# Kernel tuning notes

Hardware: AMD Instinct MI355X
Metric: run time of the kernel (lower is better)

The kernel has to match this reference:

```python
import jax, jax.numpy as jnp
import numpy as np

B, T, V = 4, 2048, 2048
D = 256   # state_dim
R = 512   # inner_dim
EPS = float(jnp.finfo(jnp.float32).eps)  # F.rms_norm default eps = dtype eps


def rms_norm(x):
    return x * jax.lax.rsqrt(jnp.mean(x * x, axis=-1, keepdims=True) + EPS)


def setup_inputs() -> dict:
    key = jax.random.key(0)
    ks = jax.random.split(key, 9)
    std = 0.02
    return {
        "x": jax.random.normal(ks[0], (B, T, V), dtype=jnp.float32),
        "Wq": jax.random.normal(ks[1], (D, V), dtype=jnp.float32) * std,
        "Wk": jax.random.normal(ks[2], (D, V), dtype=jnp.float32) * std,
        "Wv": jax.random.normal(ks[3], (D, V), dtype=jnp.float32) * std,
        "Wo": jax.random.normal(ks[4], (V, D), dtype=jnp.float32) * std,
        "decay_logit": jnp.float32(3.0),
        "q_out_scale": jnp.float32(0.1),
        "Wdown": jax.random.normal(ks[5], (R, V), dtype=jnp.float32) * std,
        "Wup": jax.random.normal(ks[6], (V, R), dtype=jnp.float32) * std,
        "t_bias": jnp.zeros((R,), dtype=jnp.float32),
        "t_out_scale": jnp.float32(0.1),
        "q_scale": jnp.ones((1,), dtype=jnp.float32),
        "t_scale": jnp.ones((1,), dtype=jnp.float32),
    }


def qtable(x, Wq, Wk, Wv, Wo, decay_logit, out_scale):
    # x: (B,T,V)
    q = jnp.einsum('btv,dv->btd', x, Wq)
    k = jnp.einsum('btv,dv->btd', x, Wk)
    v = jnp.einsum('btv,dv->btd', x, Wv)
    scores = jnp.einsum('btd,bsd->bts', q, k)  # (B,T,T)
    decay = jax.nn.sigmoid(decay_logit)
    pos = jnp.arange(T)
    diff = pos[None, :] - pos[:, None]  # diff[t,s] = s - t ... matches torch (unsqueeze(0)-unsqueeze(1))
    causal = (diff > 0).astype(jnp.float32)
    weights = decay ** jnp.clip(diff.astype(jnp.float32) - 1.0, 0.0, None) * causal
    scores = scores * weights[None, :, :]
    retrieved = jnp.einsum('bts,bsd->btd', scores, v)
    return jnp.einsum('btd,vd->btv', retrieved, Wo) * out_scale


def transform(x, Wdown, Wup, bias, out_scale):
    h = jnp.einsum('btv,rv->btr', x, Wdown) + bias
    h = jax.nn.gelu(h, approximate=False)
    return jnp.einsum('btr,vr->btv', h, Wup) * out_scale


def reference(x, Wq, Wk, Wv, Wo, decay_logit, q_out_scale,
              Wdown, Wup, t_bias, t_out_scale, q_scale, t_scale):
    x = x + q_scale * qtable(rms_norm(x), Wq, Wk, Wv, Wo, decay_logit, q_out_scale)
    x = x + t_scale * transform(rms_norm(x), Wdown, Wup, t_bias, t_out_scale)
    return x
```

## Files before the change

kernel.cpp:

```cpp
#include <hip/hip_runtime.h>
#include <cmath>

typedef _Float16 f16;
typedef _Float16 f16x8 __attribute__((ext_vector_type(8)));
typedef _Float16 f16x4 __attribute__((ext_vector_type(4)));
typedef float f32x4 __attribute__((ext_vector_type(4)));

#define MFMA16(a, b, c) __builtin_amdgcn_mfma_f32_16x16x32_f16(a, b, c, 0, 0, 0)

static constexpr int Bsz = 4;
static constexpr int T = 2048;
static constexpr int V = 2048;
static constexpr int D = 256;
static constexpr int R = 512;
static constexpr int M = Bsz * T;

__device__ __forceinline__ void load_lds16(const f16* g, f16* l) {
    __builtin_amdgcn_global_load_lds(
        (const __attribute__((address_space(1))) unsigned int*)(unsigned long long)g,
        (__attribute__((address_space(3))) unsigned int*)(unsigned int)(unsigned long long)l,
        16, 0, 0);
}

__global__ __launch_bounds__(256) void conv_all(const float* __restrict__ s0,
                                                const float* __restrict__ s1,
                                                const float* __restrict__ s2,
                                                const float* __restrict__ s3,
                                                const float* __restrict__ s4,
                                                const float* __restrict__ s5,
                                                f16* __restrict__ dst) {
    int idx = (blockIdx.x * 256 + threadIdx.x) * 4;
    if (idx >= 4194304) return;
    const float* src; int off;
    if      (idx <  524288) { src = s0; off = idx; }
    else if (idx < 1048576) { src = s1; off = idx - 524288; }
    else if (idx < 1572864) { src = s2; off = idx - 1048576; }
    else if (idx < 2097152) { src = s3; off = idx - 1572864; }
    else if (idx < 3145728) { src = s4; off = idx - 2097152; }
    else                    { src = s5; off = idx - 3145728; }
    float4 v = *(const float4*)&src[off];
    f16x4 o;
    o[0] = (f16)v.x; o[1] = (f16)v.y; o[2] = (f16)v.z; o[3] = (f16)v.w;
    *(f16x4*)&dst[idx] = o;
}

__global__ __launch_bounds__(256) void rmsnorm_kernel(const float* __restrict__ x,
                                                      f16* __restrict__ out) {
    int row = blockIdx.x;
    const float* xr = x + (size_t)row * V;
    int tid = threadIdx.x;
    float4 v0 = ((const float4*)xr)[tid];
    float4 v1 = ((const float4*)xr)[tid + 256];
    float ss = v0.x * v0.x + v0.y * v0.y + v0.z * v0.z + v0.w * v0.w
             + v1.x * v1.x + v1.y * v1.y + v1.z * v1.z + v1.w * v1.w;
    #pragma unroll
    for (int o = 32; o > 0; o >>= 1) ss += __shfl_xor(ss, o);
    __shared__ float wsum[4];
    if ((tid & 63) == 0) wsum[tid >> 6] = ss;
    __syncthreads();
    float tot = wsum[0] + wsum[1] + wsum[2] + wsum[3];
    float s = rsqrtf(tot / (float)V + 1.1920929e-07f);
    f16* orow = out + (size_t)row * V;
    f16x4 o0, o1;
    o0[0] = (f16)(v0.x * s); o0[1] = (f16)(v0.y * s);
    o0[2] = (f16)(v0.z * s); o0[3] = (f16)(v0.w * s);
    o1[0] = (f16)(v1.x * s); o1[1] = (f16)(v1.y * s);
    o1[2] = (f16)(v1.z * s); o1[3] = (f16)(v1.w * s);
    *(f16x4*)&orow[tid * 4] = o0;
    *(f16x4*)&orow[1024 + tid * 4] = o1;
}

__global__ __launch_bounds__(256) void rmsnorm_f16(const f16* __restrict__ x,
                                                   f16* __restrict__ out) {
    int row = blockIdx.x;
    int tid = threadIdx.x;
    const f16* xr = x + (size_t)row * V;
    f16x8 v = *(const f16x8*)&xr[tid * 8];
    float f[8];
    float ss = 0.f;
    #pragma unroll
    for (int j = 0; j < 8; j++) { f[j] = (float)v[j]; ss += f[j] * f[j]; }
    #pragma unroll
    for (int o = 32; o > 0; o >>= 1) ss += __shfl_xor(ss, o);
    __shared__ float wsum[4];
    if ((tid & 63) == 0) wsum[tid >> 6] = ss;
    __syncthreads();
    float tot = wsum[0] + wsum[1] + wsum[2] + wsum[3];
    float s = rsqrtf(tot / (float)V + 1.1920929e-07f);
    f16x8 o;
    #pragma unroll
    for (int j = 0; j < 8; j++) o[j] = (f16)(f[j] * s);
    *(f16x8*)&out[(size_t)row * V + tid * 8] = o;
}

struct GemmEpi {
    const float* residf;
    const f16* residh;
    float* outf;
    f16* outh;
    f16* out_q; f16* out_k; f16* out_vT;
    f16* out_h;
    const float* bias;
    const float* sA; const float* sB;
};

template <int MODE>
__global__ __launch_bounds__(256) void gemm_nt(const f16* __restrict__ A,
                                               const f16* __restrict__ Bm,
                                               int K, GemmEpi e) {
    __shared__ f16 Asl[2][128 * 32];
    __shared__ f16 Bsl[2][128 * 32];
    int tid = threadIdx.x;
    int lane = tid & 63, wv = tid >> 6;
    int wm = wv >> 1, wn = wv & 1;
    int quad = lane >> 4, l16 = lane & 15;
    int m0 = blockIdx.x * 128, n0 = blockIdx.y * 128;
    f32x4 acc[4][4] = {};

    int srow = lane >> 2;
    int scg = (lane & 3) ^ ((lane >> 3) & 3);
    const f16* Ag0 = &A[(size_t)(m0 + 16 * wv + srow) * K + scg * 8];
    const f16* Ag1 = &A[(size_t)(m0 + 16 * (wv + 4) + srow) * K + scg * 8];
    const f16* Bg0 = &Bm[(size_t)(n0 + 16 * wv + srow) * K + scg * 8];
    const f16* Bg1 = &Bm[(size_t)(n0 + 16 * (wv + 4) + srow) * K + scg * 8];
    int lo0 = (16 * wv) * 32, lo1 = (16 * (wv + 4)) * 32;

    int fs = quad ^ ((l16 >> 1) & 3);
    int niter = K >> 5;

    load_lds16(Ag0, &Asl[0][lo0]);
    load_lds16(Ag1, &Asl[0][lo1]);
    load_lds16(Bg0, &Bsl[0][lo0]);
    load_lds16(Bg1, &Bsl[0][lo1]);

    for (int i = 0; i < niter; i++) {
        int cur = i & 1;
        __builtin_amdgcn_s_barrier();
        if (i + 1 < niter) {
            int k0 = (i + 1) << 5;
            int nb = cur ^ 1;
            load_lds16(Ag0 + k0, &Asl[nb][lo0]);
            load_lds16(Ag1 + k0, &Asl[nb][lo1]);
            load_lds16(Bg0 + k0, &Bsl[nb][lo0]);
            load_lds16(Bg1 + k0, &Bsl[nb][lo1]);
            asm volatile("s_waitcnt vmcnt(4)" ::: "memory");
        } else {
            asm volatile("s_waitcnt vmcnt(0)" ::: "memory");
        }
        __builtin_amdgcn_s_barrier();
        f16x8 af[4], bf[4];
        #pragma unroll
        for (int j = 0; j < 4; j++)
            af[j] = *(const f16x8*)&Asl[cur][(64 * wm + 16 * j + l16) * 32 + fs * 8];
        #pragma unroll
        for (int j = 0; j < 4; j++)
            bf[j] = *(const f16x8*)&Bsl[cur][(64 * wn + 16 * j + l16) * 32 + fs * 8];
        #pragma unroll
        for (int mi = 0; mi < 4; mi++)
            #pragma unroll
            for (int ni = 0; ni < 4; ni++)
                acc[mi][ni] = MFMA16(af[mi], bf[ni], acc[mi][ni]);
    }

    float s = 0.f;
    if (MODE == 1 || MODE == 3) s = e.sA[0] * e.sB[0];
    #pragma unroll
    for (int mi = 0; mi < 4; mi++) {
        #pragma unroll
        for (int ni = 0; ni < 4; ni++) {
            int ml = 64 * wm + 16 * mi + quad * 4;
            int nl = 64 * wn + 16 * ni + l16;
            int gn = n0 + nl;
            #pragma unroll
            for (int i = 0; i < 4; i++) {
                int gm = m0 + ml + i;
                float vv = acc[mi][ni][i];
                if (MODE == 0) {
                    if (gn < 256) {
                        e.out_q[(size_t)gm * D + gn] = (f16)vv;
                    } else if (gn < 512) {
                        e.out_k[(size_t)gm * D + (gn - 256)] = (f16)vv;
                    } else {
                        int d = gn - 512;
                        int b = gm >> 11, t = gm & 2047;
                        e.out_vT[((size_t)b * D + d) * T + t] = (f16)vv;
                    }
                } else if (MODE == 1) {
                    size_t o = (size_t)gm * V + gn;
                    e.outh[o] = (f16)(e.residf[o] + s * vv);
                } else if (MODE == 2) {
                    float z = vv + e.bias[gn];
                    float g = 0.5f * z * (1.f + erff(z * 0.70710678118654752f));
                    e.out_h[(size_t)gm * R + gn] = (f16)g;
                } else {
                    size_t o = (size_t)gm * V + gn;
                    e.outf[o] = (float)e.residh[o] + s * vv;
                }
            }
        }
    }
}

__global__ __launch_bounds__(256) void attn_kernel(const f16* __restrict__ q,
                                                   const f16* __restrict__ k,
                                                   const f16* __restrict__ vT,
                                                   f16* __restrict__ ret,
                                                   const float* __restrict__ decay_logit) {
    __shared__ f16 Ksl[64 * 264];
    __shared__ f16 Psl[64 * 72];
    int tid = threadIdx.x, lane = tid & 63, wv = tid >> 6;
    int quad = lane >> 4, l16 = lane & 15;
    int b = blockIdx.y, t0 = blockIdx.x * 64;
    const f16* qb = q + (size_t)b * T * D;
    const f16* kb = k + (size_t)b * T * D;
    const f16* vb = vT + (size_t)b * D * T;
    f16* rb = ret + (size_t)b * T * D;

    float dl = decay_logit[0];
    float decay = 1.f / (1.f + expf(-dl));
    float l2d = log2f(decay);
    float nl2d = -l2d;

    int tq = t0 + 16 * wv + l16;
    f16x8 qf[8];
    #pragma unroll
    for (int kk = 0; kk < 8; kk++)
        qf[kk] = *(const f16x8*)&qb[(size_t)tq * D + kk * 32 + quad * 8];

    f32x4 acc2[4][4] = {};

    for (int s0 = t0; s0 < T; s0 += 64) {
        if ((float)(s0 - t0 - 64) * nl2d > 25.f) break;
        __syncthreads();
        #pragma unroll
        for (int p = 0; p < 8; p++) {
            int e0 = p * 2048 + tid * 8;
            int rr = e0 >> 8, cc = e0 & 255;
            *(f16x8*)&Ksl[rr * 264 + cc] = *(const f16x8*)&kb[(size_t)(s0 + rr) * D + cc];
        }
        __syncthreads();
        f32x4 sacc[4] = {};
        #pragma unroll
        for (int ni = 0; ni < 4; ni++) {
            #pragma unroll
            for (int kk = 0; kk < 8; kk++) {
                f16x8 bf = *(const f16x8*)&Ksl[(16 * ni + l16) * 264 + kk * 32 + quad * 8];
                sacc[ni] = MFMA16(qf[kk], bf, sacc[ni]);
            }
        }
        #pragma unroll
        for (int ni = 0; ni < 4; ni++) {
            int s_ = s0 + 16 * ni + l16;
            #pragma unroll
            for (int i = 0; i < 4; i++) {
                int t_ = t0 + 16 * wv + quad * 4 + i;
                int diff = s_ - t_;
                float w = (diff > 0) ? exp2f((float)(diff - 1) * l2d) : 0.f;
                Psl[(16 * wv + quad * 4 + i) * 72 + 16 * ni + l16] = (f16)(sacc[ni][i] * w);
            }
        }
        __syncthreads();
        #pragma unroll
        for (int kk = 0; kk < 2; kk++) {
            f16x8 pa[4], vf[4];
            #pragma unroll
            for (int mi = 0; mi < 4; mi++)
                pa[mi] = *(const f16x8*)&Psl[(16 * mi + l16) * 72 + kk * 32 + quad * 8];
            #pragma unroll
            for (int ni = 0; ni < 4; ni++)
                vf[ni] = *(const f16x8*)&vb[(size_t)(64 * wv + 16 * ni + l16) * T + s0 + kk * 32 + quad * 8];
            #pragma unroll
            for (int mi = 0; mi < 4; mi++)
                #pragma unroll
                for (int ni = 0; ni < 4; ni++)
                    acc2[mi][ni] = MFMA16(pa[mi], vf[ni], acc2[mi][ni]);
        }
    }

    #pragma unroll
    for (int mi = 0; mi < 4; mi++) {
        #pragma unroll
        for (int ni = 0; ni < 4; ni++) {
            int t_ = t0 + 16 * mi + quad * 4;
            int d_ = 64 * wv + 16 * ni + l16;
            #pragma unroll
            for (int i = 0; i < 4; i++)
                rb[(size_t)(t_ + i) * D + d_] = (f16)acc2[mi][ni][i];
        }
    }
}

extern "C" void kernel_launch(void* const* d_in, const int* in_sizes, int n_in,
                              void* d_out, int out_size, void* d_ws, size_t ws_size,
                              hipStream_t stream) {
    const float* x           = (const float*)d_in[0];
    const float* Wq          = (const float*)d_in[1];
    const float* Wk          = (const float*)d_in[2];
    const float* Wv          = (const float*)d_in[3];
    const float* Wo          = (const float*)d_in[4];
    const float* decay_logit = (const float*)d_in[5];
    const float* q_out_scale = (const float*)d_in[6];
    const float* Wdown       = (const float*)d_in[7];
    const float* Wup         = (const float*)d_in[8];
    const float* t_bias      = (const float*)d_in[9];
    const float* t_out_scale = (const float*)d_in[10];
    const float* q_scale     = (const float*)d_in[11];
    const float* t_scale     = (const float*)d_in[12];

    char* ws = (char*)d_ws;
    f16* Wqkv16  = (f16*)ws;  ws += (size_t)768 * V * 2;
    f16* Wo16    = (f16*)ws;  ws += (size_t)V * D * 2;
    f16* Wdown16 = (f16*)ws;  ws += (size_t)R * V * 2;
    f16* Wup16   = (f16*)ws;  ws += (size_t)V * R * 2;
    f16* xn16    = (f16*)ws;  ws += (size_t)M * V * 2;
    f16* q16     = (f16*)ws;  ws += (size_t)M * D * 2;
    f16* k16     = (f16*)ws;  ws += (size_t)M * D * 2;
    f16* vT16    = (f16*)ws;  ws += (size_t)Bsz * D * T * 2;
    f16* ret16   = (f16*)ws;  ws += (size_t)M * D * 2;
    f16* x2_16   = (f16*)ws;  ws += (size_t)M * V * 2;
    f16* h16     = q16;

    float* out = (float*)d_out;

    conv_all<<<dim3(4096), 256, 0, stream>>>(Wq, Wk, Wv, Wo, Wdown, Wup, Wqkv16);

    rmsnorm_kernel<<<dim3(M), 256, 0, stream>>>(x, xn16);

    {
        GemmEpi e = {};
        e.out_q = q16; e.out_k = k16; e.out_vT = vT16;
        gemm_nt<0><<<dim3(M / 128, 768 / 128), 256, 0, stream>>>(xn16, Wqkv16, V, e);
    }

    attn_kernel<<<dim3(T / 64, Bsz), 256, 0, stream>>>(q16, k16, vT16, ret16, decay_logit);

    {
        GemmEpi e = {};
        e.residf = x; e.outh = x2_16; e.sA = q_scale; e.sB = q_out_scale;
        gemm_nt<1><<<dim3(M / 128, V / 128), 256, 0, stream>>>(ret16, Wo16, D, e);
    }

    rmsnorm_f16<<<dim3(M), 256, 0, stream>>>(x2_16, xn16);

    {
        GemmEpi e = {};
        e.out_h = h16; e.bias = t_bias;
        gemm_nt<2><<<dim3(M / 128, R / 128), 256, 0, stream>>>(xn16, Wdown16, V, e);
    }

    {
        GemmEpi e = {};
        e.residh = x2_16; e.outf = out; e.sA = t_scale; e.sB = t_out_scale;
        gemm_nt<3><<<dim3(M / 128, V / 128), 256, 0, stream>>>(h16, Wup16, R, e);
    }
}
```

Before: 325.5 us.

## Split attention over key halves and use 64-row GEMM tiles for narrow GEMMs

The attention kernel gets a second grid dimension that splits the key range into two interleaved halves. Each half writes its partial result into its own 256-column slice of a 512-wide buffer, and the output projection sums the two by running with K=512 against a duplicated Wo. The QKV and down-projection GEMMs switch to a 64-row tile kernel, which doubles the number of blocks and should improve GPU occupancy for these narrow-N GEMMs. The cost is an extra duplication kernel, more workspace, doubled K in the Wo GEMM, and smaller tiles with less data reuse.

```diff
diff --git a/kernel.cpp b/kernel.cpp
--- a/kernel.cpp
+++ b/kernel.cpp
@@ -44,6 +44,13 @@
     *(f16x4*)&dst[idx] = o;
 }
 
+__global__ __launch_bounds__(256) void dup_wo(const f16* __restrict__ Wo16,
+                                              f16* __restrict__ Wodup) {
+    int idx = (blockIdx.x * 256 + threadIdx.x) * 8;
+    int n = idx >> 9, c = idx & 511;
+    *(f16x8*)&Wodup[idx] = *(const f16x8*)&Wo16[n * 256 + (c & 255)];
+}
+
 __global__ __launch_bounds__(256) void rmsnorm_kernel(const float* __restrict__ x,
                                                       f16* __restrict__ out) {
     int row = blockIdx.x;
@@ -105,6 +112,31 @@
 };
 
 template <int MODE>
+__device__ __forceinline__ void epi_store(const GemmEpi& e, float s, int gm, int gn, float vv) {
+    if (MODE == 0) {
+        if (gn < 256) {
+            e.out_q[(size_t)gm * D + gn] = (f16)vv;
+        } else if (gn < 512) {
+            e.out_k[(size_t)gm * D + (gn - 256)] = (f16)vv;
+        } else {
+            int d = gn - 512;
+            int b = gm >> 11, t = gm & 2047;
+            e.out_vT[((size_t)b * D + d) * T + t] = (f16)vv;
+        }
+    } else if (MODE == 1) {
+        size_t o = (size_t)gm * V + gn;
+        e.outh[o] = (f16)(e.residf[o] + s * vv);
+    } else if (MODE == 2) {
+        float z = vv + e.bias[gn];
+        float g = 0.5f * z * (1.f + erff(z * 0.70710678118654752f));
+        e.out_h[(size_t)gm * R + gn] = (f16)g;
+    } else {
+        size_t o = (size_t)gm * V + gn;
+        e.outf[o] = (float)e.residh[o] + s * vv;
+    }
+}
+
+template <int MODE>
 __global__ __launch_bounds__(256) void gemm_nt(const f16* __restrict__ A,
                                                const f16* __restrict__ Bm,
                                                int K, GemmEpi e) {
@@ -165,56 +197,99 @@
     float s = 0.f;
     if (MODE == 1 || MODE == 3) s = e.sA[0] * e.sB[0];
     #pragma unroll
-    for (int mi = 0; mi < 4; mi++) {
+    for (int mi = 0; mi < 4; mi++)
         #pragma unroll
         for (int ni = 0; ni < 4; ni++) {
             int ml = 64 * wm + 16 * mi + quad * 4;
             int nl = 64 * wn + 16 * ni + l16;
-            int gn = n0 + nl;
-            #pragma unroll
-            for (int i = 0; i < 4; i++) {
-                int gm = m0 + ml + i;
-                float vv = acc[mi][ni][i];
-                if (MODE == 0) {
-                    if (gn < 256) {
-                        e.out_q[(size_t)gm * D + gn] = (f16)vv;
-                    } else if (gn < 512) {
-                        e.out_k[(size_t)gm * D + (gn - 256)] = (f16)vv;
-                    } else {
-                        int d = gn - 512;
-                        int b = gm >> 11, t = gm & 2047;
-                        e.out_vT[((size_t)b * D + d) * T + t] = (f16)vv;
-                    }
-                } else if (MODE == 1) {
-                    size_t o = (size_t)gm * V + gn;
-                    e.outh[o] = (f16)(e.residf[o] + s * vv);
-                } else if (MODE == 2) {
-                    float z = vv + e.bias[gn];
-                    float g = 0.5f * z * (1.f + erff(z * 0.70710678118654752f));
-                    e.out_h[(size_t)gm * R + gn] = (f16)g;
-                } else {
-                    size_t o = (size_t)gm * V + gn;
-                    e.outf[o] = (float)e.residh[o] + s * vv;
-                }
-            }
-        }
-    }
+            #pragma unroll
+            for (int i = 0; i < 4; i++)
+                epi_store<MODE>(e, s, m0 + ml + i, n0 + nl, acc[mi][ni][i]);
+        }
+}
+
+template <int MODE>
+__global__ __launch_bounds__(256) void gemm64_nt(const f16* __restrict__ A,
+                                                 const f16* __restrict__ Bm,
+                                                 int K, GemmEpi e) {
+    __shared__ f16 Asl[2][64 * 32];
+    __shared__ f16 Bsl[2][128 * 32];
+    int tid = threadIdx.x;
+    int lane = tid & 63, wv = tid >> 6;
+    int quad = lane >> 4, l16 = lane & 15;
+    int m0 = blockIdx.x * 64, n0 = blockIdx.y * 128;
+    f32x4 acc[4][2] = {};
+
+    int srow = lane >> 2;
+    int scg = (lane & 3) ^ ((lane >> 3) & 3);
+    const f16* Ag0 = &A[(size_t)(m0 + 16 * wv + srow) * K + scg * 8];
+    const f16* Bg0 = &Bm[(size_t)(n0 + 16 * wv + srow) * K + scg * 8];
+    const f16* Bg1 = &Bm[(size_t)(n0 + 16 * (wv + 4) + srow) * K + scg * 8];
+    int lo0 = (16 * wv) * 32, lo1 = (16 * (wv + 4)) * 32;
+
+    int fs = quad ^ ((l16 >> 1) & 3);
+    int niter = K >> 5;
+
+    load_lds16(Ag0, &Asl[0][lo0]);
+    load_lds16(Bg0, &Bsl[0][lo0]);
+    load_lds16(Bg1, &Bsl[0][lo1]);
+
+    for (int i = 0; i < niter; i++) {
+        int cur = i & 1;
+        __builtin_amdgcn_s_barrier();
+        if (i + 1 < niter) {
+            int k0 = (i + 1) << 5;
+            int nb = cur ^ 1;
+            load_lds16(Ag0 + k0, &Asl[nb][lo0]);
+            load_lds16(Bg0 + k0, &Bsl[nb][lo0]);
+            load_lds16(Bg1 + k0, &Bsl[nb][lo1]);
+            asm volatile("s_waitcnt vmcnt(3)" ::: "memory");
+        } else {
+            asm volatile("s_waitcnt vmcnt(0)" ::: "memory");
+        }
+        __builtin_amdgcn_s_barrier();
+        f16x8 af[4], bf[2];
+        #pragma unroll
+        for (int j = 0; j < 4; j++)
+            af[j] = *(const f16x8*)&Asl[cur][(16 * j + l16) * 32 + fs * 8];
+        #pragma unroll
+        for (int j = 0; j < 2; j++)
+            bf[j] = *(const f16x8*)&Bsl[cur][(32 * wv + 16 * j + l16) * 32 + fs * 8];
+        #pragma unroll
+        for (int mi = 0; mi < 4; mi++)
+            #pragma unroll
+            for (int ni = 0; ni < 2; ni++)
+                acc[mi][ni] = MFMA16(af[mi], bf[ni], acc[mi][ni]);
+    }
+
+    float s = 0.f;
+    if (MODE == 1 || MODE == 3) s = e.sA[0] * e.sB[0];
+    #pragma unroll
+    for (int mi = 0; mi < 4; mi++)
+        #pragma unroll
+        for (int ni = 0; ni < 2; ni++) {
+            int ml = 16 * mi + quad * 4;
+            int nl = 32 * wv + 16 * ni + l16;
+            #pragma unroll
+            for (int i = 0; i < 4; i++)
+                epi_store<MODE>(e, s, m0 + ml + i, n0 + nl, acc[mi][ni][i]);
+        }
 }
 
 __global__ __launch_bounds__(256) void attn_kernel(const f16* __restrict__ q,
                                                    const f16* __restrict__ k,
                                                    const f16* __restrict__ vT,
-                                                   f16* __restrict__ ret,
+                                                   f16* __restrict__ ret2,
                                                    const float* __restrict__ decay_logit) {
     __shared__ f16 Ksl[64 * 264];
     __shared__ f16 Psl[64 * 72];
     int tid = threadIdx.x, lane = tid & 63, wv = tid >> 6;
     int quad = lane >> 4, l16 = lane & 15;
-    int b = blockIdx.y, t0 = blockIdx.x * 64;
+    int b = blockIdx.y, t0 = blockIdx.x * 64, z = blockIdx.z;
     const f16* qb = q + (size_t)b * T * D;
     const f16* kb = k + (size_t)b * T * D;
     const f16* vb = vT + (size_t)b * D * T;
-    f16* rb = ret + (size_t)b * T * D;
+    f16* rb = ret2 + (size_t)b * T * 512 + z * 256;
 
     float dl = decay_logit[0];
     float decay = 1.f / (1.f + expf(-dl));
@@ -229,7 +304,7 @@
 
     f32x4 acc2[4][4] = {};
 
-    for (int s0 = t0; s0 < T; s0 += 64) {
+    for (int s0 = t0 + 64 * z; s0 < T; s0 += 128) {
         if ((float)(s0 - t0 - 64) * nl2d > 25.f) break;
         __syncthreads();
         #pragma unroll
@@ -285,7 +360,7 @@
             int d_ = 64 * wv + 16 * ni + l16;
             #pragma unroll
             for (int i = 0; i < 4; i++)
-                rb[(size_t)(t_ + i) * D + d_] = (f16)acc2[mi][ni][i];
+                rb[(size_t)(t_ + i) * 512 + d_] = (f16)acc2[mi][ni][i];
         }
     }
 }
@@ -312,32 +387,34 @@
     f16* Wo16    = (f16*)ws;  ws += (size_t)V * D * 2;
     f16* Wdown16 = (f16*)ws;  ws += (size_t)R * V * 2;
     f16* Wup16   = (f16*)ws;  ws += (size_t)V * R * 2;
+    f16* Wodup   = (f16*)ws;  ws += (size_t)V * 512 * 2;
     f16* xn16    = (f16*)ws;  ws += (size_t)M * V * 2;
     f16* q16     = (f16*)ws;  ws += (size_t)M * D * 2;
     f16* k16     = (f16*)ws;  ws += (size_t)M * D * 2;
     f16* vT16    = (f16*)ws;  ws += (size_t)Bsz * D * T * 2;
-    f16* ret16   = (f16*)ws;  ws += (size_t)M * D * 2;
+    f16* ret2    = (f16*)ws;  ws += (size_t)M * 512 * 2;
     f16* x2_16   = (f16*)ws;  ws += (size_t)M * V * 2;
     f16* h16     = q16;
 
     float* out = (float*)d_out;
 
     conv_all<<<dim3(4096), 256, 0, stream>>>(Wq, Wk, Wv, Wo, Wdown, Wup, Wqkv16);
+    dup_wo<<<dim3(512), 256, 0, stream>>>(Wo16, Wodup);
 
     rmsnorm_kernel<<<dim3(M), 256, 0, stream>>>(x, xn16);
 
     {
         GemmEpi e = {};
         e.out_q = q16; e.out_k = k16; e.out_vT = vT16;
-        gemm_nt<0><<<dim3(M / 128, 768 / 128), 256, 0, stream>>>(xn16, Wqkv16, V, e);
-    }
-
-    attn_kernel<<<dim3(T / 64, Bsz), 256, 0, stream>>>(q16, k16, vT16, ret16, decay_logit);
+        gemm64_nt<0><<<dim3(M / 64, 768 / 128), 256, 0, stream>>>(xn16, Wqkv16, V, e);
+    }
+
+    attn_kernel<<<dim3(T / 64, Bsz, 2), 256, 0, stream>>>(q16, k16, vT16, ret2, decay_logit);
 
     {
         GemmEpi e = {};
         e.residf = x; e.outh = x2_16; e.sA = q_scale; e.sB = q_out_scale;
-        gemm_nt<1><<<dim3(M / 128, V / 128), 256, 0, stream>>>(ret16, Wo16, D, e);
+        gemm_nt<1><<<dim3(M / 128, V / 128), 256, 0, stream>>>(ret2, Wodup, 512, e);
     }
 
     rmsnorm_f16<<<dim3(M), 256, 0, stream>>>(x2_16, xn16);
@@ -345,7 +422,7 @@
     {
         GemmEpi e = {};
         e.out_h = h16; e.bias = t_bias;
-        gemm_nt<2><<<dim3(M / 128, R / 128), 256, 0, stream>>>(xn16, Wdown16, V, e);
+        gemm64_nt<2><<<dim3(M / 64, R / 128), 256, 0, stream>>>(xn16, Wdown16, V, e);
     }
 
     {
```

Result: slower. 333.1 us (+2.3%).
